# Kernel optimization log

Hardware: AMD Instinct MI355X
Metric: run time of the kernel (lower is better)

The kernel has to match this reference:

```python
import jax, jax.numpy as jnp
import numpy as np

B, H, W, D, DFF = 32, 40, 40, 128, 2048
S = H * W  # 1600
BN_EPS = 1e-5


def setup_inputs() -> dict:
    key = jax.random.key(0)
    ks = jax.random.split(key, 8)
    se = jax.random.normal(ks[2], (H, W, H, W), dtype=jnp.float32)
    se = se + jnp.transpose(se, (2, 3, 0, 1))  # symmetric init as in torch code
    wscale = 0.02
    return {
        "tgt": jax.random.normal(ks[0], (B, H, W, D), dtype=jnp.float32),
        "memory": jax.random.normal(ks[1], (B, H, W, D), dtype=jnp.float32),
        "score_embed": se,
        "w1": jax.random.normal(ks[3], (D, D), dtype=jnp.float32) * wscale,
        "b1": jnp.zeros((D,), jnp.float32),
        "g1": jnp.ones((2 * S,), jnp.float32),
        "be1": jnp.zeros((2 * S,), jnp.float32),
        "w2": jax.random.normal(ks[4], (DFF, 2 * S), dtype=jnp.float32) * wscale,
        "b2": jnp.zeros((DFF,), jnp.float32),
        "g2": jnp.ones((DFF,), jnp.float32),
        "be2": jnp.zeros((DFF,), jnp.float32),
        "w3": jax.random.normal(ks[5], (1, DFF), dtype=jnp.float32) * wscale,
        "b3": jnp.zeros((1,), jnp.float32),
        "g3": jnp.ones((1,), jnp.float32),
        "be3": jnp.zeros((1,), jnp.float32),
    }


def _bn_eval(x, gamma, beta):
    # BatchNorm eval mode with running_mean=0, running_var=1 (as initialized)
    return x * (gamma / jnp.sqrt(1.0 + BN_EPS)) + beta


def _l2norm(x):
    # F.normalize(p=2, dim=-1) with eps=1e-12
    return x / jnp.maximum(jnp.linalg.norm(x, axis=-1, keepdims=True), 1e-12)


def reference(tgt, memory, score_embed, w1, b1, g1, be1, w2, b2, g2, be2, w3, b3, g3, be3):
    b, h, w, d = tgt.shape
    s = h * w
    q = _l2norm(tgt.reshape(b, s, d) @ w1.T + b1)   # [B,S,D]
    k = _l2norm(memory.reshape(b, s, d) @ w1.T + b1)
    gate = jax.nn.sigmoid(score_embed.reshape(s, s))  # [S,S]
    attn = jnp.einsum("bsd,btd->bst", q, k) * gate    # [B,S,S]
    m1 = attn.max(axis=1)  # max over dim 1 -> [B,S]
    m2 = attn.max(axis=2)  # max over dim 2 -> [B,S]
    x = jnp.concatenate([m1, m2], axis=1)  # [B,2S]
    x = _bn_eval(x, g1, be1)
    x = x @ w2.T + b2        # [B,DFF]
    x = jax.nn.relu(_bn_eval(x, g2, be2))
    x = x @ w3.T + b3        # [B,1]
    x = _bn_eval(x, g3, be3)
    return x.squeeze(-1)     # [B]
```

## Files before the change

kernel.cpp:

```cpp
#include <hip/hip_runtime.h>
#include <hip/hip_bf16.h>

#define BB 32
#define SS 1600
#define DD 128
#define DFFN 2048
#define S2N 3200
#define RS 136

typedef __attribute__((ext_vector_type(8))) short short8;
typedef __attribute__((ext_vector_type(4))) float floatx4;
typedef unsigned int u32;
typedef unsigned short u16;

__device__ __forceinline__ u32 encf(float f) {
  u32 u = __float_as_uint(f);
  return (u & 0x80000000u) ? ~u : (u | 0x80000000u);
}
__device__ __forceinline__ float decf(u32 e) {
  u32 u = (e & 0x80000000u) ? (e & 0x7fffffffu) : ~e;
  return __uint_as_float(u);
}
__device__ __forceinline__ u16 f2b(float x) {
  __hip_bfloat16 h = __float2bfloat16(x);
  return __builtin_bit_cast(u16, h);
}
__device__ __forceinline__ float sigm(float x) { return 1.f / (1.f + __expf(-x)); }
__device__ __forceinline__ short8 pack8(float4 a, float4 b) {
  short8 r;
  r[0] = (short)f2b(a.x); r[1] = (short)f2b(a.y); r[2] = (short)f2b(a.z); r[3] = (short)f2b(a.w);
  r[4] = (short)f2b(b.x); r[5] = (short)f2b(b.y); r[6] = (short)f2b(b.z); r[7] = (short)f2b(b.w);
  return r;
}

__global__ __launch_bounds__(256) void k_prep(const float* __restrict__ tgt,
                                              const float* __restrict__ memin,
                                              const float* __restrict__ w1,
                                              const float* __restrict__ b1,
                                              const float* __restrict__ se,
                                              u16* __restrict__ qb, u16* __restrict__ kb,
                                              u16* __restrict__ gT2,
                                              u32* __restrict__ m1u, u32* __restrict__ m2u) {
  __shared__ u16 sA[128 * RS];
  __shared__ float sq[128];
  int tid = threadIdx.x;
  int lane = tid & 63, wv = tid >> 6;
  int wr = wv >> 1, wc = wv & 1;
  int l15 = lane & 15, lg = lane >> 4;

  if (blockIdx.x >= 800) {
    int bid = blockIdx.x - 800;
    int ii = bid * 256 + tid;
    if (ii < BB * SS) {
      m1u[ii] = 0u;
      m2u[ii] = 0u;
    }
    int r2 = bid >> 2, mi = bid & 3;
    int sy = r2 / 13, tx = r2 - sy * 13;
    int s0 = min(sy * 128, SS - 128);
    int t0 = min(tx * 128, SS - 128);
    int srow = s0 + wr * 64 + mi * 16 + lg * 4;
    u16* tb = gT2 + (size_t)r2 * 16384 + wv * 4096 + lane * 8;
    for (int ni = 0; ni < 4; ++ni) {
      int tcol = t0 + wc * 64 + ni * 16 + l15;
      const float* sp = se + (size_t)srow * SS + tcol;
      ushort4 o;
      o.x = f2b(sigm(sp[0]));
      o.y = f2b(sigm(sp[SS]));
      o.z = f2b(sigm(sp[2 * SS]));
      o.w = f2b(sigm(sp[3 * SS]));
      *(ushort4*)(tb + (mi * 2 + (ni >> 1)) * 512 + (ni & 1) * 4) = o;
    }
    return;
  }

  long row0 = (long)blockIdx.x * 128;
  const float* src;
  u16* dst;
  if (row0 < (long)BB * SS) { src = tgt + row0 * DD; dst = qb + row0 * DD; }
  else { src = memin + (row0 - (long)BB * SS) * DD; dst = kb + (row0 - (long)BB * SS) * DD; }

  for (int p = 0; p < 16; ++p) {
    int r = p * 8 + (tid >> 5);
    int c4 = (tid & 31) * 4;
    float4 v = *(const float4*)(src + r * DD + c4);
    u32 p0 = (u32)f2b(v.x) | ((u32)f2b(v.y) << 16);
    u32 p1 = (u32)f2b(v.z) | ((u32)f2b(v.w) << 16);
    *(u32*)&sA[r * RS + c4] = p0;
    *(u32*)&sA[r * RS + c4 + 2] = p1;
  }
  if (tid < 128) sq[tid] = 0.f;
  __syncthreads();

  floatx4 acc[4][4];
  for (int mi = 0; mi < 4; ++mi)
    for (int ni = 0; ni < 4; ++ni) acc[mi][ni] = (floatx4){0.f, 0.f, 0.f, 0.f};

  for (int kc = 0; kc < 4; ++kc) {
    int k0 = kc * 32 + lg * 8;
    short8 af[4], bfr[4];
    for (int mi = 0; mi < 4; ++mi) af[mi] = *(const short8*)&sA[(wr * 64 + mi * 16 + l15) * RS + k0];
    for (int ni = 0; ni < 4; ++ni) {
      const float* wp = w1 + (size_t)(wc * 64 + ni * 16 + l15) * DD + k0;
      bfr[ni] = pack8(*(const float4*)wp, *(const float4*)(wp + 4));
    }
    for (int mi = 0; mi < 4; ++mi)
      for (int ni = 0; ni < 4; ++ni)
        acc[mi][ni] = __builtin_amdgcn_mfma_f32_16x16x32_bf16(af[mi], bfr[ni], acc[mi][ni], 0, 0, 0);
  }

  float bvals[4];
  for (int ni = 0; ni < 4; ++ni) bvals[ni] = b1[wc * 64 + ni * 16 + l15];
  for (int mi = 0; mi < 4; ++mi)
    for (int r = 0; r < 4; ++r) {
      float s = 0.f;
      for (int ni = 0; ni < 4; ++ni) {
        float v = acc[mi][ni][r] + bvals[ni];
        acc[mi][ni][r] = v;
        s += v * v;
      }
      s += __shfl_xor(s, 1); s += __shfl_xor(s, 2);
      s += __shfl_xor(s, 4); s += __shfl_xor(s, 8);
      if (l15 == 0) atomicAdd(&sq[wr * 64 + mi * 16 + lg * 4 + r], s);
    }
  __syncthreads();

  for (int mi = 0; mi < 4; ++mi)
    for (int r = 0; r < 4; ++r) {
      int row = wr * 64 + mi * 16 + lg * 4 + r;
      float scale = 1.f / fmaxf(sqrtf(sq[row]), 1e-12f);
      for (int ni = 0; ni < 4; ++ni)
        sA[row * RS + wc * 64 + ni * 16 + l15] = f2b(acc[mi][ni][r] * scale);
    }
  __syncthreads();
  for (int p = 0; p < 16; ++p) {
    int r = p * 8 + (tid >> 5);
    int c4 = (tid & 31) * 4;
    uint2 val = *(const uint2*)&sA[r * RS + c4];
    *(uint2*)(dst + r * DD + c4) = val;
  }
}

__global__ __launch_bounds__(256, 4) void k_attn(const u16* __restrict__ qb,
                                                 const u16* __restrict__ kb,
                                                 const u16* __restrict__ gT2,
                                                 u32* __restrict__ m1u, u32* __restrict__ m2u) {
  __shared__ u16 sK[128 * RS];
  __shared__ float scmax[2][128];
  __shared__ float srmax[2][128];
  int tid = threadIdx.x;
  int n = blockIdx.x;
  int m = n >> 3;
  int r2 = m >> 2;
  int b = (n & 7) * 4 + (m & 3);
  int sy = r2 / 13, tx = r2 - sy * 13;
  int s0 = min(sy * 128, SS - 128);
  int t0 = min(tx * 128, SS - 128);
  int lane = tid & 63, wv = tid >> 6;
  int wr = wv >> 1, wc = wv & 1;
  int l15 = lane & 15, lg = lane >> 4;
  const size_t base = (size_t)b * SS * DD;
  const u16* qp = qb + base + (size_t)(s0 + wr * 64 + l15) * DD + lg * 8;

  {
    int rr0 = tid >> 4;
    int c8 = (tid & 15) * 8;
    const u16* kp = kb + base + (size_t)(t0 + rr0) * DD + c8;
    u16* sp = &sK[rr0 * RS + c8];
    for (int p = 0; p < 8; ++p)
      *(uint4*)(sp + p * 16 * RS) = *(const uint4*)(kp + (size_t)p * 16 * DD);
  }
  short8 qsA[4], qsB[4];
  for (int mi = 0; mi < 4; ++mi) qsA[mi] = *(const short8*)(qp + mi * 16 * DD);
  __syncthreads();

  floatx4 acc[4][4];
  for (int mi = 0; mi < 4; ++mi)
    for (int ni = 0; ni < 4; ++ni) acc[mi][ni] = (floatx4){0.f, 0.f, 0.f, 0.f};

#define QKSTEP(KC, CUR, NXT, PRE)                                                     \
  {                                                                                   \
    if (PRE)                                                                          \
      for (int mi = 0; mi < 4; ++mi)                                                  \
        NXT[mi] = *(const short8*)(qp + mi * 16 * DD + ((KC) + 1) * 32);              \
    int k0 = (KC)*32 + lg * 8;                                                        \
    short8 bfr[4];                                                                    \
    for (int ni = 0; ni < 4; ++ni)                                                    \
      bfr[ni] = *(const short8*)&sK[(wc * 64 + ni * 16 + l15) * RS + k0];             \
    for (int mi = 0; mi < 4; ++mi)                                                    \
      for (int ni = 0; ni < 4; ++ni)                                                  \
        acc[mi][ni] = __builtin_amdgcn_mfma_f32_16x16x32_bf16(CUR[mi], bfr[ni],       \
                                                              acc[mi][ni], 0, 0, 0);  \
  }
  QKSTEP(0, qsA, qsB, 1)
  QKSTEP(1, qsB, qsA, 1)
  QKSTEP(2, qsA, qsB, 1)
  QKSTEP(3, qsB, qsA, 0)
#undef QKSTEP

  uint4 g4[8];
  {
    const u16* gbase = gT2 + (size_t)r2 * 16384 + wv * 4096 + lane * 8;
    for (int p = 0; p < 8; ++p) g4[p] = *(const uint4*)(gbase + p * 512);
  }

  float rmax[4][4];
  for (int mi = 0; mi < 4; ++mi)
    for (int r = 0; r < 4; ++r) rmax[mi][r] = -1e30f;
  float cmax[4];
  for (int ni = 0; ni < 4; ++ni) cmax[ni] = -1e30f;

  for (int mi = 0; mi < 4; ++mi)
    for (int ni = 0; ni < 4; ++ni) {
      uint4 pg = g4[mi * 2 + (ni >> 1)];
      u32 lo = (ni & 1) ? pg.z : pg.x;
      u32 hi = (ni & 1) ? pg.w : pg.y;
      float v0 = acc[mi][ni][0] * __uint_as_float(lo << 16);
      float v1 = acc[mi][ni][1] * __uint_as_float(lo & 0xffff0000u);
      float v2 = acc[mi][ni][2] * __uint_as_float(hi << 16);
      float v3 = acc[mi][ni][3] * __uint_as_float(hi & 0xffff0000u);
      rmax[mi][0] = fmaxf(rmax[mi][0], v0);
      rmax[mi][1] = fmaxf(rmax[mi][1], v1);
      rmax[mi][2] = fmaxf(rmax[mi][2], v2);
      rmax[mi][3] = fmaxf(rmax[mi][3], v3);
      cmax[ni] = fmaxf(cmax[ni], fmaxf(fmaxf(v0, v1), fmaxf(v2, v3)));
    }

  for (int ni = 0; ni < 4; ++ni) {
    cmax[ni] = fmaxf(cmax[ni], __shfl_xor(cmax[ni], 16));
    cmax[ni] = fmaxf(cmax[ni], __shfl_xor(cmax[ni], 32));
  }
  if (lane < 16)
    for (int ni = 0; ni < 4; ++ni) scmax[wr][wc * 64 + ni * 16 + lane] = cmax[ni];

  for (int mi = 0; mi < 4; ++mi)
    for (int r = 0; r < 4; ++r) {
      float v = rmax[mi][r];
      v = fmaxf(v, __shfl_xor(v, 1));
      v = fmaxf(v, __shfl_xor(v, 2));
      v = fmaxf(v, __shfl_xor(v, 4));
      v = fmaxf(v, __shfl_xor(v, 8));
      if (l15 == 0) srmax[wc][wr * 64 + mi * 16 + lg * 4 + r] = v;
    }
  __syncthreads();

  if (tid < 128) {
    float v = fmaxf(scmax[0][tid], scmax[1][tid]);
    atomicMax(&m1u[b * SS + t0 + tid], encf(v));
  } else {
    int i2 = tid - 128;
    float v = fmaxf(srmax[0][i2], srmax[1][i2]);
    atomicMax(&m2u[b * SS + s0 + i2], encf(v));
  }
}

__global__ __launch_bounds__(256) void k_gemm2(const u32* __restrict__ m1u,
                                               const u32* __restrict__ m2u,
                                               const float* __restrict__ g1,
                                               const float* __restrict__ be1,
                                               const float* __restrict__ w2,
                                               float* __restrict__ hacc) {
  int tid = threadIdx.x;
  int lane = tid & 63, wv = tid >> 6;
  int f0 = blockIdx.x * 32 + wv * 8;
  int cs = blockIdx.y;
  int cr0 = cs * 400;
  const u32* msrc = (cs < 4) ? m1u : m2u;
  int mcol0 = cr0 - ((cs < 4) ? 0 : SS);
  int c_sub = lane & 15, bq = lane >> 4;
  const float bnc = rsqrtf(1.f + 1e-5f);
  float acc[8][8];
  for (int a = 0; a < 8; ++a)
    for (int c = 0; c < 8; ++c) acc[a][c] = 0.f;
  const float4 z4 = {0.f, 0.f, 0.f, 0.f};
  for (int it = 0; it < 7; ++it) {
    int coff = it * 64 + c_sub * 4;
    bool ok = coff < 400;
    int cg = cr0 + coff;
    float4 w4[8], x4[8];
    float4 gv = ok ? *(const float4*)(g1 + cg) : z4;
    float4 bv = ok ? *(const float4*)(be1 + cg) : z4;
    gv.x *= bnc; gv.y *= bnc; gv.z *= bnc; gv.w *= bnc;
    for (int jf = 0; jf < 8; ++jf)
      w4[jf] = ok ? *(const float4*)(w2 + (size_t)(f0 + jf) * S2N + cg) : z4;
    for (int j = 0; j < 8; ++j) {
      if (ok) {
        uint4 e = *(const uint4*)(msrc + (size_t)(bq * 8 + j) * SS + mcol0 + coff);
        x4[j].x = decf(e.x) * gv.x + bv.x;
        x4[j].y = decf(e.y) * gv.y + bv.y;
        x4[j].z = decf(e.z) * gv.z + bv.z;
        x4[j].w = decf(e.w) * gv.w + bv.w;
      } else {
        x4[j] = z4;
      }
    }
    for (int jf = 0; jf < 8; ++jf)
      for (int j = 0; j < 8; ++j) {
        float a = acc[jf][j];
        a = fmaf(w4[jf].x, x4[j].x, a);
        a = fmaf(w4[jf].y, x4[j].y, a);
        a = fmaf(w4[jf].z, x4[j].z, a);
        a = fmaf(w4[jf].w, x4[j].w, a);
        acc[jf][j] = a;
      }
  }
  for (int jf = 0; jf < 8; ++jf)
    for (int j = 0; j < 8; ++j) {
      float v = acc[jf][j];
      v += __shfl_xor(v, 1); v += __shfl_xor(v, 2);
      v += __shfl_xor(v, 4); v += __shfl_xor(v, 8);
      acc[jf][j] = v;
    }
  if ((lane & 15) == 0) {
    for (int jf = 0; jf < 8; ++jf)
      for (int j = 0; j < 8; ++j) {
        int b = bq * 8 + j;
        hacc[((size_t)cs * BB + b) * DFFN + f0 + jf] = acc[jf][j];
      }
  }
}

__global__ __launch_bounds__(256) void k_final(const float* __restrict__ hacc,
                                               const float* __restrict__ b2,
                                               const float* __restrict__ g2,
                                               const float* __restrict__ be2,
                                               const float* __restrict__ w3,
                                               const float* __restrict__ b3,
                                               const float* __restrict__ g3,
                                               const float* __restrict__ be3,
                                               float* __restrict__ out) {
  __shared__ float wsum[4];
  int b = blockIdx.x;
  int tid = threadIdx.x;
  float bnc = rsqrtf(1.f + 1e-5f);
  float part = 0.f;
  for (int f = tid; f < DFFN; f += 256) {
    float s = b2[f];
    for (int cs = 0; cs < 8; ++cs) s += hacc[((size_t)cs * BB + b) * DFFN + f];
    s = s * (g2[f] * bnc) + be2[f];
    s = fmaxf(s, 0.f);
    part += s * w3[f];
  }
  for (int m = 1; m < 64; m <<= 1) part += __shfl_xor(part, m);
  if ((tid & 63) == 0) wsum[tid >> 6] = part;
  __syncthreads();
  if (tid == 0) {
    float tot = wsum[0] + wsum[1] + wsum[2] + wsum[3] + b3[0];
    out[b] = tot * (g3[0] * bnc) + be3[0];
  }
}

extern "C" void kernel_launch(void* const* d_in, const int* in_sizes, int n_in,
                              void* d_out, int out_size, void* d_ws, size_t ws_size,
                              hipStream_t stream) {
  const float* tgt = (const float*)d_in[0];
  const float* memin = (const float*)d_in[1];
  const float* se = (const float*)d_in[2];
  const float* w1 = (const float*)d_in[3];
  const float* b1 = (const float*)d_in[4];
  const float* g1 = (const float*)d_in[5];
  const float* be1 = (const float*)d_in[6];
  const float* w2 = (const float*)d_in[7];
  const float* b2 = (const float*)d_in[8];
  const float* g2 = (const float*)d_in[9];
  const float* be2 = (const float*)d_in[10];
  const float* w3 = (const float*)d_in[11];
  const float* b3 = (const float*)d_in[12];
  const float* g3 = (const float*)d_in[13];
  const float* be3 = (const float*)d_in[14];
  float* out = (float*)d_out;

  char* ws = (char*)d_ws;
  const size_t OFF_GT = 0;
  const size_t OFF_QB = 5537792;
  const size_t OFF_KB = OFF_QB + 13107200;
  const size_t OFF_M1 = OFF_KB + 13107200;
  const size_t OFF_M2 = OFF_M1 + 204800;
  const size_t OFF_HA = OFF_M2 + 204800;
  const size_t NEEDED = OFF_HA + 2097152;
  if (ws_size < NEEDED) return;

  u16* gT2 = (u16*)(ws + OFF_GT);
  u16* qb = (u16*)(ws + OFF_QB);
  u16* kb = (u16*)(ws + OFF_KB);
  u32* m1u = (u32*)(ws + OFF_M1);
  u32* m2u = (u32*)(ws + OFF_M2);
  float* hacc = (float*)(ws + OFF_HA);

  k_prep<<<1476, 256, 0, stream>>>(tgt, memin, w1, b1, se, qb, kb, gT2, m1u, m2u);
  k_attn<<<5408, 256, 0, stream>>>(qb, kb, gT2, m1u, m2u);
  k_gemm2<<<dim3(64, 8), 256, 0, stream>>>(m1u, m2u, g1, be1, w2, hacc);
  k_final<<<32, 256, 0, stream>>>(hacc, b2, g2, be2, w3, b3, g3, be3, out);
}
```

Measured before the change: 144.1 us.

## Load K fragments directly from global into registers, dropping LDS staging in attn

The QK^T kernel no longer stages the K tile in shared memory. Each wave loads its K MFMA operands straight from global memory into double-buffered registers, the same way Q is already loaded, which removes the LDS write/read round trip and a __syncthreads. The gate load is moved ahead of the last MFMA step so it overlaps compute. The occupancy hint drops from 4 to 3 blocks per CU to make room for the extra registers, and K rows are now re-read from global/L2 by both wave rows instead of once per block.

```diff
diff --git a/kernel.cpp b/kernel.cpp
--- a/kernel.cpp
+++ b/kernel.cpp
@@ -141,11 +141,10 @@
   }
 }
 
-__global__ __launch_bounds__(256, 4) void k_attn(const u16* __restrict__ qb,
+__global__ __launch_bounds__(256, 3) void k_attn(const u16* __restrict__ qb,
                                                  const u16* __restrict__ kb,
                                                  const u16* __restrict__ gT2,
                                                  u32* __restrict__ m1u, u32* __restrict__ m2u) {
-  __shared__ u16 sK[128 * RS];
   __shared__ float scmax[2][128];
   __shared__ float srmax[2][128];
   int tid = threadIdx.x;
@@ -161,48 +160,40 @@
   int l15 = lane & 15, lg = lane >> 4;
   const size_t base = (size_t)b * SS * DD;
   const u16* qp = qb + base + (size_t)(s0 + wr * 64 + l15) * DD + lg * 8;
-
-  {
-    int rr0 = tid >> 4;
-    int c8 = (tid & 15) * 8;
-    const u16* kp = kb + base + (size_t)(t0 + rr0) * DD + c8;
-    u16* sp = &sK[rr0 * RS + c8];
-    for (int p = 0; p < 8; ++p)
-      *(uint4*)(sp + p * 16 * RS) = *(const uint4*)(kp + (size_t)p * 16 * DD);
-  }
-  short8 qsA[4], qsB[4];
+  const u16* kp = kb + base + (size_t)(t0 + wc * 64 + l15) * DD + lg * 8;
+
+  short8 qsA[4], qsB[4], ksA[4], ksB[4];
   for (int mi = 0; mi < 4; ++mi) qsA[mi] = *(const short8*)(qp + mi * 16 * DD);
-  __syncthreads();
+  for (int ni = 0; ni < 4; ++ni) ksA[ni] = *(const short8*)(kp + ni * 16 * DD);
 
   floatx4 acc[4][4];
   for (int mi = 0; mi < 4; ++mi)
     for (int ni = 0; ni < 4; ++ni) acc[mi][ni] = (floatx4){0.f, 0.f, 0.f, 0.f};
 
-#define QKSTEP(KC, CUR, NXT, PRE)                                                     \
+  uint4 g4[8];
+
+#define QKSTEP(KC, QC, KCUR, QN, KN, PRE)                                             \
   {                                                                                   \
-    if (PRE)                                                                          \
+    if (PRE) {                                                                        \
       for (int mi = 0; mi < 4; ++mi)                                                  \
-        NXT[mi] = *(const short8*)(qp + mi * 16 * DD + ((KC) + 1) * 32);              \
-    int k0 = (KC)*32 + lg * 8;                                                        \
-    short8 bfr[4];                                                                    \
-    for (int ni = 0; ni < 4; ++ni)                                                    \
-      bfr[ni] = *(const short8*)&sK[(wc * 64 + ni * 16 + l15) * RS + k0];             \
+        QN[mi] = *(const short8*)(qp + mi * 16 * DD + ((KC) + 1) * 32);               \
+      for (int ni = 0; ni < 4; ++ni)                                                  \
+        KN[ni] = *(const short8*)(kp + ni * 16 * DD + ((KC) + 1) * 32);               \
+    }                                                                                 \
     for (int mi = 0; mi < 4; ++mi)                                                    \
       for (int ni = 0; ni < 4; ++ni)                                                  \
-        acc[mi][ni] = __builtin_amdgcn_mfma_f32_16x16x32_bf16(CUR[mi], bfr[ni],       \
+        acc[mi][ni] = __builtin_amdgcn_mfma_f32_16x16x32_bf16(QC[mi], KCUR[ni],       \
                                                               acc[mi][ni], 0, 0, 0);  \
   }
-  QKSTEP(0, qsA, qsB, 1)
-  QKSTEP(1, qsB, qsA, 1)
-  QKSTEP(2, qsA, qsB, 1)
-  QKSTEP(3, qsB, qsA, 0)
-#undef QKSTEP
-
-  uint4 g4[8];
+  QKSTEP(0, qsA, ksA, qsB, ksB, 1)
+  QKSTEP(1, qsB, ksB, qsA, ksA, 1)
+  QKSTEP(2, qsA, ksA, qsB, ksB, 1)
   {
     const u16* gbase = gT2 + (size_t)r2 * 16384 + wv * 4096 + lane * 8;
     for (int p = 0; p < 8; ++p) g4[p] = *(const uint4*)(gbase + p * 512);
   }
+  QKSTEP(3, qsB, ksB, qsA, ksA, 0)
+#undef QKSTEP
 
   float rmax[4][4];
   for (int mi = 0; mi < 4; ++mi)
```

Result: slower. 178.7 us (+24.0%).
